# Kernel optimization log

Hardware: AMD Instinct MI355X
Metric: run time of the kernel (lower is better)

Reference implementation:

```python
import jax, jax.numpy as jnp
import numpy as np

B, S, DIM = 1, 2048, 2048
NH, NKV, HD = 32, 8, 64
NREP = NH // NKV
SCALE = 1.0 / float(np.sqrt(HD))
NEG = -1e30


def _apply_rope(q, k, rope_cache):
    # q: (B,S,NH,HD), k: (B,S,NKV,HD); rope_cache: (S, HD) = [cos | sin], each HD//2 wide
    cos = rope_cache[:, : HD // 2][None, :, None, :]  # (1,S,1,HD/2)
    sin = rope_cache[:, HD // 2 :][None, :, None, :]

    def rot(x):
        x1, x2 = x[..., : HD // 2], x[..., HD // 2 :]
        return jnp.concatenate([x1 * cos - x2 * sin, x1 * sin + x2 * cos], axis=-1)

    return rot(q), rot(k)


def setup_inputs() -> dict:
    key = jax.random.key(0)
    ks = jax.random.split(key, 12)
    std = 0.02
    x = jax.random.normal(ks[0], (B, S, DIM), jnp.float32)
    # real rotary cos/sin cache
    inv_freq = 1.0 / (10000.0 ** (np.arange(0, HD, 2, dtype=np.float64) / HD))
    freqs = np.outer(np.arange(S, dtype=np.float64), inv_freq)
    rope_cache = jnp.asarray(
        np.concatenate([np.cos(freqs), np.sin(freqs)], axis=-1), jnp.float32
    )  # (S, HD)
    return {
        "x": x,
        "rope_cache": rope_cache,
        "wq_w": jax.random.normal(ks[1], (NH * HD, DIM), jnp.float32) * std,
        "wq_b": jax.random.normal(ks[2], (NH * HD,), jnp.float32) * std,
        "wk_w": jax.random.normal(ks[3], (NKV * HD, DIM), jnp.float32) * std,
        "wk_b": jax.random.normal(ks[4], (NKV * HD,), jnp.float32) * std,
        "wv_w": jax.random.normal(ks[5], (NKV * HD, DIM), jnp.float32) * std,
        "wv_b": jax.random.normal(ks[6], (NKV * HD,), jnp.float32) * std,
        "wo_w": jax.random.normal(ks[7], (DIM, NH * HD), jnp.float32) * std,
        "wo_b": jax.random.normal(ks[8], (DIM,), jnp.float32) * std,
        "sinks": jax.random.normal(ks[9], (NH,), jnp.float32) * std,
    }


def reference(x, rope_cache, wq_w, wq_b, wk_w, wk_b, wv_w, wv_b, wo_w, wo_b, sinks):
    q = (x @ wq_w.T + wq_b).reshape(B, S, NH, HD)
    k = (x @ wk_w.T + wk_b).reshape(B, S, NKV, HD)
    v = (x @ wv_w.T + wv_b).reshape(B, S, NKV, HD)
    q, k = _apply_rope(q, k, rope_cache)
    q = q.transpose(0, 2, 1, 3)  # (B,NH,S,HD)
    k = jnp.repeat(k.transpose(0, 2, 1, 3), NREP, axis=1)  # GQA expand -> (B,NH,S,HD)
    v = jnp.repeat(v.transpose(0, 2, 1, 3), NREP, axis=1)
    scores = jnp.einsum("bhqd,bhkd->bhqk", q, k) * SCALE
    causal = jnp.tril(jnp.ones((S, S), bool))
    scores = jnp.where(causal[None, None], scores, NEG)
    lse = jax.scipy.special.logsumexp(scores, axis=-1)  # (B,NH,S)
    attn = jnp.exp(scores - lse[..., None])
    out = jnp.einsum("bhqk,bhkd->bhqd", attn, v)
    sink_scale = jax.nn.sigmoid(lse - sinks[None, :, None])  # (B,NH,S)
    out = out * sink_scale[..., None]
    out = out.transpose(0, 2, 1, 3).reshape(B, S, NH * HD)
    return out @ wo_w.T + wo_b
```

## Files before the change

kernel.cpp:

```cpp
#include <hip/hip_runtime.h>

typedef unsigned short ushort_t;
typedef short s8v __attribute__((ext_vector_type(8)));
typedef float f4v __attribute__((ext_vector_type(4)));

#define DIMK   2048
#define NHEAD  32
#define HDIM   64
#define SCALE_LOG2E 0.18033688f

__device__ __forceinline__ unsigned short f2bf(float f) {
    unsigned u = __float_as_uint(f);
    u += 0x7fffu + ((u >> 16) & 1u);
    return (unsigned short)(u >> 16);
}

__device__ __forceinline__ unsigned pack_bf2(float f0, float f1) {
    unsigned a = __float_as_uint(f0) + 0x8000u;
    unsigned b = __float_as_uint(f1) + 0x8000u;
    return __builtin_amdgcn_perm(b, a, 0x07060302u);
}

__device__ __forceinline__ float fexp2(float x) {
#if __has_builtin(__builtin_amdgcn_exp2f)
    return __builtin_amdgcn_exp2f(x);
#else
    return exp2f(x);
#endif
}

__device__ __forceinline__ void gll16(const void* g, void* l) {
    __builtin_amdgcn_global_load_lds(
        (const __attribute__((address_space(1))) void*)g,
        (__attribute__((address_space(3))) void*)l, 16, 0, 0);
}

__device__ __forceinline__ f4v mfma16(s8v a, s8v b, f4v c) {
    return __builtin_amdgcn_mfma_f32_16x16x32_bf16(a, b, c, 0, 0, 0);
}

__global__ __launch_bounds__(256) void cast_all(
    const float* __restrict__ x,  const float* __restrict__ wq,
    const float* __restrict__ wk, const float* __restrict__ wv,
    const float* __restrict__ wo,
    ushort_t* __restrict__ xb,  ushort_t* __restrict__ wqb,
    ushort_t* __restrict__ wkb, ushort_t* __restrict__ wvb,
    ushort_t* __restrict__ wob)
{
    int i = blockIdx.x * 256 + threadIdx.x;
    const float* src; ushort_t* dst;
    if      (i < 1048576) { src = x;  dst = xb; }
    else if (i < 2097152) { src = wq; dst = wqb; i -= 1048576; }
    else if (i < 2359296) { src = wk; dst = wkb; i -= 2097152; }
    else if (i < 2621440) { src = wv; dst = wvb; i -= 2359296; }
    else                  { src = wo; dst = wob; i -= 2621440; }
    float4 v = ((const float4*)src)[i];
    ushort4 o;
    o.x = f2bf(v.x); o.y = f2bf(v.y); o.z = f2bf(v.z); o.w = f2bf(v.w);
    ((ushort4*)dst)[i] = o;
}

__device__ __forceinline__ void gemm_core64(
    const ushort_t* __restrict__ A, const ushort_t* __restrict__ Bt,
    int bm, int bn64, ushort_t* As, ushort_t* Bs, f4v acc[2][4])
{
    const int tid  = threadIdx.x;
    const int wave = tid >> 6, lane = tid & 63;
    const int c = lane & 15, q4 = lane >> 4;
    const int lrow = lane >> 3;
    const int lchunk = (lane & 7) ^ lrow;

    const ushort_t* ag = A  + (size_t)(bm * 128 + wave * 32 + lrow) * DIMK + lchunk * 8;
    const ushort_t* bg = Bt + (size_t)(bn64 * 64 + wave * 16 + lrow) * DIMK + lchunk * 8;
    ushort_t* asw = As + (wave * 32) * 64;
    ushort_t* bsw = Bs + (wave * 16) * 64;

    const int Ra = wave * 32 + c;
    for (int k0 = 0; k0 < DIMK; k0 += 64) {
        gll16(ag + k0,             asw);
        gll16(ag +  8 * DIMK + k0, asw + 512);
        gll16(ag + 16 * DIMK + k0, asw + 1024);
        gll16(ag + 24 * DIMK + k0, asw + 1536);
        gll16(bg + k0,             bsw);
        gll16(bg +  8 * DIMK + k0, bsw + 512);
        __syncthreads();
        s8v af[2][2], bfv[4][2];
#pragma unroll
        for (int mt = 0; mt < 2; ++mt)
#pragma unroll
            for (int kc = 0; kc < 2; ++kc) {
                int R = Ra + mt * 16;
                af[mt][kc] = *(const s8v*)(As + (R * 8 + ((kc * 4 + q4) ^ (R & 7))) * 8);
            }
#pragma unroll
        for (int nt = 0; nt < 4; ++nt)
#pragma unroll
            for (int kc = 0; kc < 2; ++kc) {
                int R = nt * 16 + c;
                bfv[nt][kc] = *(const s8v*)(Bs + (R * 8 + ((kc * 4 + q4) ^ (R & 7))) * 8);
            }
#pragma unroll
        for (int kc = 0; kc < 2; ++kc)
#pragma unroll
            for (int mt = 0; mt < 2; ++mt)
#pragma unroll
                for (int nt = 0; nt < 4; ++nt)
                    acc[mt][nt] = mfma16(af[mt][kc], bfv[nt][kc], acc[mt][nt]);
        __syncthreads();
    }
}

__global__ __launch_bounds__(256) void qkv_gemm(
    const ushort_t* __restrict__ Xb,
    const ushort_t* __restrict__ Wqb, const ushort_t* __restrict__ Wkb, const ushort_t* __restrict__ Wvb,
    const float* __restrict__ biasq, const float* __restrict__ biask, const float* __restrict__ biasv,
    const float* __restrict__ rope,
    ushort_t* __restrict__ Qo, ushort_t* __restrict__ Kblk, ushort_t* __restrict__ Vblk)
{
    __shared__ ushort_t SM[12288];
    ushort_t* As = SM;
    ushort_t* Bs = SM + 8192;
    const int nb = blockIdx.x, bm = blockIdx.y;
    const ushort_t* Bt; const float* bias; int nbl, mode;
    if      (nb < 32) { Bt = Wqb; bias = biasq; nbl = nb;      mode = 0; }
    else if (nb < 40) { Bt = Wkb; bias = biask; nbl = nb - 32; mode = 1; }
    else              { Bt = Wvb; bias = biasv; nbl = nb - 40; mode = 2; }

    const f4v fz = {0.f, 0.f, 0.f, 0.f};
    f4v acc[2][4];
    for (int i = 0; i < 2; ++i) for (int j = 0; j < 4; ++j) acc[i][j] = fz;

    gemm_core64(Xb, Bt, bm, nbl, As, Bs, acc);

    const int tid = threadIdx.x, wave = tid >> 6, lane = tid & 63;
    const int c = lane & 15, q4 = lane >> 4;

    if (mode == 0) {
#pragma unroll
        for (int mt = 0; mt < 2; ++mt)
#pragma unroll
            for (int r = 0; r < 4; ++r) {
                int rowl = wave * 32 + mt * 16 + q4 * 4 + r;
                int row  = bm * 128 + rowl;
                const float* rp = rope + row * 64;
#pragma unroll
                for (int nt = 0; nt < 2; ++nt) {
                    int d   = nt * 16 + c;
                    int col = nbl * 64 + d;
                    float cs = rp[d], sn = rp[32 + d];
                    float x1 = acc[mt][nt][r]     + bias[col];
                    float x2 = acc[mt][nt + 2][r] + bias[col + 32];
                    SM[rowl * 64 + d]      = f2bf((x1 * cs - x2 * sn) * SCALE_LOG2E);
                    SM[rowl * 64 + d + 32] = f2bf((x1 * sn + x2 * cs) * SCALE_LOG2E);
                }
            }
    } else if (mode == 1) {
#pragma unroll
        for (int mt = 0; mt < 2; ++mt)
#pragma unroll
            for (int r = 0; r < 4; ++r) {
                int rowl = wave * 32 + mt * 16 + q4 * 4 + r;
                int row  = bm * 128 + rowl;
                const float* rp = rope + row * 64;
                int tl  = rowl >> 6;
                int ntk = (rowl & 63) >> 4, ck = rowl & 15;
#pragma unroll
                for (int nt = 0; nt < 2; ++nt) {
                    int d   = nt * 16 + c;
                    int col = nbl * 64 + d;
                    float cs = rp[d], sn = rp[32 + d];
                    float x1 = acc[mt][nt][r]     + bias[col];
                    float x2 = acc[mt][nt + 2][r] + bias[col + 32];
                    float o1 = x1 * cs - x2 * sn;
                    float o2 = x1 * sn + x2 * cs;
                    {   int dd = d;       int kc = dd >> 5, q4k = (dd >> 3) & 3, j = dd & 7;
                        SM[tl * 4096 + ((kc * 4 + ntk) * 64 + q4k * 16 + ck) * 8 + j] = f2bf(o1); }
                    {   int dd = d + 32;  int kc = dd >> 5, q4k = (dd >> 3) & 3, j = dd & 7;
                        SM[tl * 4096 + ((kc * 4 + ntk) * 64 + q4k * 16 + ck) * 8 + j] = f2bf(o2); }
                }
            }
    } else {
#pragma unroll
        for (int mt = 0; mt < 2; ++mt)
#pragma unroll
            for (int nt = 0; nt < 4; ++nt)
#pragma unroll
                for (int r = 0; r < 4; ++r) {
                    int rowl = wave * 32 + mt * 16 + q4 * 4 + r;
                    int col  = nbl * 64 + nt * 16 + c;
                    int tl = rowl >> 6, K64 = rowl & 63;
                    int kp = (K64 & 15) * 4 + (K64 >> 4);
                    int kc = kp >> 5, q4v = (kp >> 3) & 3, j = kp & 7;
                    SM[tl * 4096 + ((kc * 4 + nt) * 64 + q4v * 16 + c) * 8 + j]
                        = f2bf(acc[mt][nt][r] + bias[col]);
                }
    }
    __syncthreads();

    if (mode == 0) {
#pragma unroll
        for (int i = 0; i < 4; ++i) {
            int idx  = i * 256 + tid;
            int rowl = idx >> 3, c8 = (idx & 7) * 8;
            *(int4*)(Qo + (size_t)(bm * 128 + rowl) * 2048 + nbl * 64 + c8)
                = *(const int4*)(SM + idx * 8);
        }
    } else {
        ushort_t* dstb = (mode == 1 ? Kblk : Vblk) + ((size_t)nbl * 32 + bm * 2) * 4096;
#pragma unroll
        for (int i = 0; i < 4; ++i) {
            int idx = i * 256 + tid;
            *(int4*)(dstb + idx * 8) = *(const int4*)(SM + idx * 8);
        }
    }
}

__global__ __launch_bounds__(256) void proj_gemm(
    const ushort_t* __restrict__ Ob, const ushort_t* __restrict__ Wob,
    const float* __restrict__ bias, float* __restrict__ Co)
{
    __shared__ ushort_t SM[12288];
    ushort_t* As = SM;
    ushort_t* Bs = SM + 8192;
    const f4v fz = {0.f, 0.f, 0.f, 0.f};
    f4v acc[2][4];
    for (int i = 0; i < 2; ++i) for (int j = 0; j < 4; ++j) acc[i][j] = fz;

    gemm_core64(Ob, Wob, blockIdx.y, blockIdx.x, As, Bs, acc);

    const int tid = threadIdx.x, wave = tid >> 6, lane = tid & 63;
    const int c = lane & 15, q4 = lane >> 4;
#pragma unroll
    for (int mt = 0; mt < 2; ++mt)
#pragma unroll
        for (int nt = 0; nt < 4; ++nt)
#pragma unroll
            for (int r = 0; r < 4; ++r) {
                int row = blockIdx.y * 128 + wave * 32 + mt * 16 + q4 * 4 + r;
                int col = blockIdx.x * 64 + nt * 16 + c;
                Co[(size_t)row * 2048 + col] = acc[mt][nt][r] + bias[col];
            }
}

__global__ __launch_bounds__(256) void attn_kernel(
    const ushort_t* __restrict__ Qb,
    const ushort_t* __restrict__ Kblk,
    const ushort_t* __restrict__ Vblk,
    const float* __restrict__ sinks,
    ushort_t* __restrict__ Ob)
{
    __shared__ ushort_t Ps[4][32 * 72];
    const int p = blockIdx.x, h = blockIdx.y, kvh = h >> 2;
    const int tid = threadIdx.x, wave = tid >> 6, lane = tid & 63;
    const int c = lane & 15, q4 = lane >> 4;
    const int t  = (wave < 2) ? p : (31 - p);
    const int q0 = t * 64 + (wave & 1) * 32;
    ushort_t* Pw = &Ps[wave][0];

    s8v qf[2][2];
#pragma unroll
    for (int mi = 0; mi < 2; ++mi)
#pragma unroll
        for (int kc = 0; kc < 2; ++kc)
            qf[mi][kc] = *(const s8v*)(Qb + (size_t)(q0 + mi * 16 + c) * 2048 + h * 64 + kc * 32 + q4 * 8);

    const f4v fz = {0.f, 0.f, 0.f, 0.f};
    f4v Oacc[2][4];
    float Lp[2][4];
#pragma unroll
    for (int mi = 0; mi < 2; ++mi) {
#pragma unroll
        for (int dt = 0; dt < 4; ++dt) Oacc[mi][dt] = fz;
#pragma unroll
        for (int r = 0; r < 4; ++r) Lp[mi][r] = 0.f;
    }

    const ushort_t* kbase = Kblk + (size_t)kvh * 32 * 4096;
    const ushort_t* vbase = Vblk + (size_t)kvh * 32 * 4096;

    for (int kt = 0; kt <= t; ++kt) {
        const ushort_t* kp = kbase + (size_t)kt * 4096;
        const ushort_t* vp = vbase + (size_t)kt * 4096;
        s8v kf[4][2], vf[4][2];
#pragma unroll
        for (int kc = 0; kc < 2; ++kc)
#pragma unroll
            for (int nt = 0; nt < 4; ++nt) {
                kf[nt][kc] = *(const s8v*)(kp + ((kc * 4 + nt) * 64 + lane) * 8);
                vf[nt][kc] = *(const s8v*)(vp + ((kc * 4 + nt) * 64 + lane) * 8);
            }

        f4v S[2][4];
#pragma unroll
        for (int mi = 0; mi < 2; ++mi)
#pragma unroll
            for (int nt = 0; nt < 4; ++nt) S[mi][nt] = fz;
#pragma unroll
        for (int kc = 0; kc < 2; ++kc)
#pragma unroll
            for (int nt = 0; nt < 4; ++nt)
#pragma unroll
                for (int mi = 0; mi < 2; ++mi)
                    S[mi][nt] = mfma16(qf[mi][kc], kf[nt][kc], S[mi][nt]);

        if (kt == t) {
#pragma unroll
            for (int mi = 0; mi < 2; ++mi)
#pragma unroll
                for (int nt = 0; nt < 4; ++nt) {
                    int key = t * 64 + nt * 16 + c;
#pragma unroll
                    for (int r = 0; r < 4; ++r) {
                        int qrow = q0 + mi * 16 + q4 * 4 + r;
                        if (key > qrow) S[mi][nt][r] = -1.0e30f;
                    }
                }
        }

#pragma unroll
        for (int mi = 0; mi < 2; ++mi)
#pragma unroll
            for (int r = 0; r < 4; ++r) {
                float p0 = fexp2(S[mi][0][r]), p1 = fexp2(S[mi][1][r]);
                float p2 = fexp2(S[mi][2][r]), p3 = fexp2(S[mi][3][r]);
                Lp[mi][r] += (p0 + p1) + (p2 + p3);
                int2 w_; w_.x = (int)pack_bf2(p0, p1); w_.y = (int)pack_bf2(p2, p3);
                *(int2*)(Pw + (mi * 16 + q4 * 4 + r) * 72 + c * 4) = w_;
            }
        s8v pa[2][2];
#pragma unroll
        for (int mi = 0; mi < 2; ++mi)
#pragma unroll
            for (int kc = 0; kc < 2; ++kc)
                pa[mi][kc] = *(const s8v*)(Pw + (mi * 16 + c) * 72 + kc * 32 + q4 * 8);
#pragma unroll
        for (int kc = 0; kc < 2; ++kc)
#pragma unroll
            for (int dt = 0; dt < 4; ++dt)
#pragma unroll
                for (int mi = 0; mi < 2; ++mi)
                    Oacc[mi][dt] = mfma16(pa[mi][kc], vf[dt][kc], Oacc[mi][dt]);
    }

#pragma unroll
    for (int mi = 0; mi < 2; ++mi)
#pragma unroll
        for (int r = 0; r < 4; ++r)
#pragma unroll
            for (int off = 1; off < 16; off <<= 1)
                Lp[mi][r] += __shfl_xor(Lp[mi][r], off);

    const float sk = sinks[h];
#pragma unroll
    for (int mi = 0; mi < 2; ++mi)
#pragma unroll
        for (int r = 0; r < 4; ++r) {
            float L = Lp[mi][r];
            float lse = __logf(L);
            float sig = 1.f / (1.f + __expf(sk - lse));
            float sc  = sig / L;
            int row = q0 + mi * 16 + q4 * 4 + r;
#pragma unroll
            for (int dt = 0; dt < 4; ++dt)
                Ob[(size_t)row * 2048 + h * 64 + dt * 16 + c] = f2bf(Oacc[mi][dt][r] * sc);
        }
}

extern "C" void kernel_launch(void* const* d_in, const int* in_sizes, int n_in,
                              void* d_out, int out_size, void* d_ws, size_t ws_size,
                              hipStream_t stream)
{
    (void)in_sizes; (void)n_in; (void)out_size; (void)ws_size;
    const float* x     = (const float*)d_in[0];
    const float* rope  = (const float*)d_in[1];
    const float* wq    = (const float*)d_in[2];
    const float* qb    = (const float*)d_in[3];
    const float* wk    = (const float*)d_in[4];
    const float* kb    = (const float*)d_in[5];
    const float* wv    = (const float*)d_in[6];
    const float* vb    = (const float*)d_in[7];
    const float* wo    = (const float*)d_in[8];
    const float* wob_f = (const float*)d_in[9];
    const float* sinks = (const float*)d_in[10];
    float* out = (float*)d_out;

    char* ws = (char*)d_ws;
    ushort_t* xb   = (ushort_t*)(ws);
    ushort_t* wqb  = (ushort_t*)(ws + (8ull  << 20));
    ushort_t* wkb  = (ushort_t*)(ws + (16ull << 20));
    ushort_t* wvb  = (ushort_t*)(ws + (18ull << 20));
    ushort_t* wob  = (ushort_t*)(ws + (20ull << 20));
    ushort_t* qo   = (ushort_t*)(ws + (28ull << 20));
    ushort_t* kblk = (ushort_t*)(ws + (36ull << 20));
    ushort_t* vblk = (ushort_t*)(ws + (38ull << 20));
    ushort_t* ao   = (ushort_t*)(ws + (40ull << 20));

    cast_all<<<14336, 256, 0, stream>>>(x, wq, wk, wv, wo, xb, wqb, wkb, wvb, wob);
    qkv_gemm<<<dim3(48, 16), 256, 0, stream>>>(xb, wqb, wkb, wvb, qb, kb, vb, rope, qo, kblk, vblk);
    attn_kernel<<<dim3(16, 32), 256, 0, stream>>>(qo, kblk, vblk, sinks, ao);
    proj_gemm<<<dim3(32, 16), 256, 0, stream>>>(ao, wob, wob_f, out);
}
```

Baseline: 218.0 us.

## Share K/V tiles across GQA heads via double-buffered LDS in attention

```diff
diff --git a/kernel.cpp b/kernel.cpp
--- a/kernel.cpp
+++ b/kernel.cpp
@@ -249,12 +249,14 @@
     const float* __restrict__ sinks,
     ushort_t* __restrict__ Ob)
 {
+    __shared__ ushort_t KV[2][8192];
     __shared__ ushort_t Ps[4][32 * 72];
-    const int p = blockIdx.x, h = blockIdx.y, kvh = h >> 2;
+    const int qq = 63 - blockIdx.x, kvh = blockIdx.y;
     const int tid = threadIdx.x, wave = tid >> 6, lane = tid & 63;
     const int c = lane & 15, q4 = lane >> 4;
-    const int t  = (wave < 2) ? p : (31 - p);
-    const int q0 = t * 64 + (wave & 1) * 32;
+    const int h  = kvh * 4 + wave;
+    const int q0 = qq * 32;
+    const int nkt = (qq >> 1) + 1;
     ushort_t* Pw = &Ps[wave][0];
 
     s8v qf[2][2];
@@ -275,40 +277,50 @@
         for (int r = 0; r < 4; ++r) Lp[mi][r] = 0.f;
     }
 
-    const ushort_t* kbase = Kblk + (size_t)kvh * 32 * 4096;
-    const ushort_t* vbase = Vblk + (size_t)kvh * 32 * 4096;
-
-    for (int kt = 0; kt <= t; ++kt) {
-        const ushort_t* kp = kbase + (size_t)kt * 4096;
-        const ushort_t* vp = vbase + (size_t)kt * 4096;
-        s8v kf[4][2], vf[4][2];
+    const ushort_t* kg = Kblk + (size_t)kvh * 32 * 4096 + lane * 8;
+    const ushort_t* vg = Vblk + (size_t)kvh * 32 * 4096 + lane * 8;
+
+#define ATTN_STAGE(KT, BUF)                                                    \
+    do {                                                                       \
+        ushort_t* db_ = &KV[BUF][0];                                           \
+        _Pragma("unroll")                                                      \
+        for (int i_ = 0; i_ < 2; ++i_) {                                       \
+            int ch_ = wave * 2 + i_;                                           \
+            gll16(kg + (size_t)(KT) * 4096 + ch_ * 512, db_ + ch_ * 512);      \
+            gll16(vg + (size_t)(KT) * 4096 + ch_ * 512, db_ + 4096 + ch_ * 512); \
+        }                                                                      \
+    } while (0)
+
+    ATTN_STAGE(0, 0);
+    __syncthreads();
+
+    for (int kt = 0; kt < nkt; ++kt) {
+        const int buf = kt & 1;
+        if (kt + 1 < nkt) ATTN_STAGE(kt + 1, buf ^ 1);
+        const ushort_t* kb_ = &KV[buf][0];
+        const ushort_t* vb_ = &KV[buf][4096];
+
+        f4v S[2][4];
+#pragma unroll
+        for (int mi = 0; mi < 2; ++mi)
+#pragma unroll
+            for (int nt = 0; nt < 4; ++nt) S[mi][nt] = fz;
 #pragma unroll
         for (int kc = 0; kc < 2; ++kc)
 #pragma unroll
             for (int nt = 0; nt < 4; ++nt) {
-                kf[nt][kc] = *(const s8v*)(kp + ((kc * 4 + nt) * 64 + lane) * 8);
-                vf[nt][kc] = *(const s8v*)(vp + ((kc * 4 + nt) * 64 + lane) * 8);
-            }
-
-        f4v S[2][4];
-#pragma unroll
-        for (int mi = 0; mi < 2; ++mi)
-#pragma unroll
-            for (int nt = 0; nt < 4; ++nt) S[mi][nt] = fz;
-#pragma unroll
-        for (int kc = 0; kc < 2; ++kc)
-#pragma unroll
-            for (int nt = 0; nt < 4; ++nt)
+                s8v kf = *(const s8v*)(kb_ + ((kc * 4 + nt) * 64 + lane) * 8);
 #pragma unroll
                 for (int mi = 0; mi < 2; ++mi)
-                    S[mi][nt] = mfma16(qf[mi][kc], kf[nt][kc], S[mi][nt]);
-
-        if (kt == t) {
+                    S[mi][nt] = mfma16(qf[mi][kc], kf, S[mi][nt]);
+            }
+
+        if (kt == nkt - 1) {
 #pragma unroll
             for (int mi = 0; mi < 2; ++mi)
 #pragma unroll
                 for (int nt = 0; nt < 4; ++nt) {
-                    int key = t * 64 + nt * 16 + c;
+                    int key = kt * 64 + nt * 16 + c;
 #pragma unroll
                     for (int r = 0; r < 4; ++r) {
                         int qrow = q0 + mi * 16 + q4 * 4 + r;
@@ -333,14 +345,19 @@
 #pragma unroll
             for (int kc = 0; kc < 2; ++kc)
                 pa[mi][kc] = *(const s8v*)(Pw + (mi * 16 + c) * 72 + kc * 32 + q4 * 8);
+
 #pragma unroll
         for (int kc = 0; kc < 2; ++kc)
 #pragma unroll
-            for (int dt = 0; dt < 4; ++dt)
+            for (int dt = 0; dt < 4; ++dt) {
+                s8v vf = *(const s8v*)(vb_ + ((kc * 4 + dt) * 64 + lane) * 8);
 #pragma unroll
                 for (int mi = 0; mi < 2; ++mi)
-                    Oacc[mi][dt] = mfma16(pa[mi][kc], vf[dt][kc], Oacc[mi][dt]);
+                    Oacc[mi][dt] = mfma16(pa[mi][kc], vf, Oacc[mi][dt]);
+            }
+        __syncthreads();
     }
+#undef ATTN_STAGE
 
 #pragma unroll
     for (int mi = 0; mi < 2; ++mi)
@@ -397,6 +414,6 @@
 
     cast_all<<<14336, 256, 0, stream>>>(x, wq, wk, wv, wo, xb, wqb, wkb, wvb, wob);
     qkv_gemm<<<dim3(48, 16), 256, 0, stream>>>(xb, wqb, wkb, wvb, qb, kb, vb, rope, qo, kblk, vblk);
-    attn_kernel<<<dim3(16, 32), 256, 0, stream>>>(qo, kblk, vblk, sinks, ao);
+    attn_kernel<<<dim3(64, 8), 256, 0, stream>>>(qo, kblk, vblk, sinks, ao);
     proj_gemm<<<dim3(32, 16), 256, 0, stream>>>(ao, wob, wob_f, out);
 }
```

Measured after the change: 227.0 us. 4.2% more time.
